# Kernel tuning notes

Measured on AMD Instinct MI355X. Metric: run time of the kernel, lower is better.

The kernel has to match this reference:

```python
import jax, jax.numpy as jnp
import numpy as np


def setup_inputs() -> dict:
    key0 = jax.random.key(0)
    kq, kk, kv = jax.random.split(key0, 3)
    B, S, H, KVH, D = 1, 4096, 8, 2, 64
    return {
        "query": jax.random.normal(kq, (B, S, H, D), dtype=jnp.float32),
        "key": jax.random.normal(kk, (B, S, KVH, D), dtype=jnp.float32),
        "value": jax.random.normal(kv, (B, S, KVH, D), dtype=jnp.float32),
    }


def _ring_attn_single(query, key, value):
    # world_size == 1 (dist uninitialized): ring loop is a single local step
    # with query_offset == key_offset == 0.
    B, S, H, D = query.shape
    KVH = key.shape[2]
    scale = D ** -0.5
    # [B, H, S, D]
    q = query.transpose(0, 2, 1, 3)
    k = key.transpose(0, 2, 1, 3)
    v = value.transpose(0, 2, 1, 3)
    if KVH != H:
        rep = H // KVH
        k = jnp.repeat(k, rep, axis=1)  # repeat_interleave on head dim
        v = jnp.repeat(v, rep, axis=1)
    logits = jnp.einsum("bhqd,bhkd->bhqk", q, k) * scale
    pos = jnp.arange(S)
    causal = pos[:, None] < pos[None, :]  # mask future keys
    logits = jnp.where(causal[None, None], -jnp.inf, logits)
    w = jax.nn.softmax(logits, axis=-1)  # [B, H, S, S]
    attn_out = jnp.einsum("bhqk,bhkd->bhqd", w, v)
    cw = jnp.sum(w, axis=-1, keepdims=True)  # chunk softmax mass (== 1)
    out = attn_out * cw / (cw + 1e-8)  # weight-accumulation renorm
    return out.transpose(0, 2, 1, 3)  # [B, S, H, D]


def reference(query, key, value):
    return _ring_attn_single(query, key, value)
```

## Files before the change

kernel.cpp:

```cpp
#include <hip/hip_runtime.h>
#include <hip/hip_bf16.h>


#define S_LEN 4096
#define H_Q   8
#define H_KV  2
#define DH    64
#define BN    64
#define PITCH 72
#define NEG_BIG (-1e30f)
#define CS (0.125f * 1.44269504088896340736f)

#define CHUNK 12
#define NTR   102
#define KB_SH (S_LEN * H_KV * DH)
#define OB_FLOATS ((size_t)NTR * H_Q * 128 * DH)
#define L_FLOATS  ((size_t)NTR * H_Q * 128)
#define WS_NEED ((size_t)(2 * KB_SH) * 2 + (OB_FLOATS + L_FLOATS) * 4)

typedef __attribute__((ext_vector_type(8))) short bf16x8;
typedef __attribute__((ext_vector_type(4))) short s16x4;
typedef __attribute__((ext_vector_type(4))) float f32x4;
typedef __attribute__((ext_vector_type(4))) unsigned int u32x4;

__device__ __forceinline__ short bf(float x) {
    return __builtin_bit_cast(short, __float2bfloat16(x));
}
__device__ __forceinline__ unsigned int pk2(float lo, float hi) {
    return (unsigned int)(unsigned short)bf(lo)
         | ((unsigned int)(unsigned short)bf(hi) << 16);
}

__global__ __launch_bounds__(256)
void ring_attn_prepass(const float* __restrict__ K, const float* __restrict__ V,
                       short* __restrict__ Kb, short* __restrict__ Vt) {
    const int b = blockIdx.x;
    const int t = threadIdx.x;
    if (b < 512) {
        const int i = (b * 256 + t) * 4;
        float4 kv = *(const float4*)(K + i);
        *(unsigned int*)(Kb + i)     = pk2(kv.x, kv.y);
        *(unsigned int*)(Kb + i + 2) = pk2(kv.z, kv.w);
    } else {
        __shared__ short T[DH * PITCH];
        const int bb  = b - 512;
        const int kvh = bb >> 6;
        const int s0  = (bb & 63) * 64;
        {
            const int r  = t >> 2;
            const int dq = (t & 3) * 16;
            const float* vp = V + ((s0 + r) * H_KV + kvh) * DH + dq;
            float4 a0 = *(const float4*)(vp);
            float4 a1 = *(const float4*)(vp + 4);
            float4 a2 = *(const float4*)(vp + 8);
            float4 a3 = *(const float4*)(vp + 12);
            float e[16] = {a0.x,a0.y,a0.z,a0.w, a1.x,a1.y,a1.z,a1.w,
                           a2.x,a2.y,a2.z,a2.w, a3.x,a3.y,a3.z,a3.w};
#pragma unroll
            for (int i = 0; i < 16; ++i)
                T[(dq + i) * PITCH + r] = bf(e[i]);
        }
        __syncthreads();
        {
            const int d = t >> 2;
            const int q = t & 3;
            s16x4 g0 = *(const s16x4*)(&T[d * PITCH + 4 * q]);
            s16x4 g1 = *(const s16x4*)(&T[d * PITCH + 16 + 4 * q]);
            s16x4 g2 = *(const s16x4*)(&T[d * PITCH + 32 + 4 * q]);
            s16x4 g3 = *(const s16x4*)(&T[d * PITCH + 48 + 4 * q]);
            bf16x8 x0 = bf16x8{g0[0],g0[1],g0[2],g0[3], g1[0],g1[1],g1[2],g1[3]};
            bf16x8 x1 = bf16x8{g2[0],g2[1],g2[2],g2[3], g3[0],g3[1],g3[2],g3[3]};
            short* op = Vt + (kvh * DH + d) * S_LEN + s0 + 16 * q;
            *(bf16x8*)(op)     = x0;
            *(bf16x8*)(op + 8) = x1;
        }
    }
}

template <bool SPLIT>
__global__ __launch_bounds__(256, 4)
void ring_attn_fwd(const float* __restrict__ Q, const short* __restrict__ Kb,
                   const short* __restrict__ Vt, float* __restrict__ O,
                   float* __restrict__ Obuf, float* __restrict__ Lbuf) {
    const int bid = blockIdx.x;
    const int h   = bid & 7;
    int qt, nch, jbeg, jend, tr0;
    if (SPLIT) {
        const int tr = (NTR - 1) - (bid >> 3);
        int b, base;
        if (tr < 6)       { b = 0; base = 0; }
        else if (tr < 18) { b = 1; base = 6; }
        else if (tr < 36) { b = 2; base = 18; }
        else if (tr < 60) { b = 3; base = 36; }
        else if (tr < 90) { b = 4; base = 60; }
        else              { b = 5; base = 90; }
        const int u  = tr - base;
        const int qq = u / (b + 1);
        const int ch = u - qq * (b + 1);
        qt   = 6 * b + qq;
        nch  = b + 1;
        tr0  = base + qq * (b + 1);
        jbeg = ch * CHUNK;
        jend = min(2 * qt + 2, jbeg + CHUNK);
    } else {
        qt = 31 - (bid >> 3);
        nch = 1; jbeg = 0; jend = 2 * qt + 2; tr0 = 0;
    }
    const int kvh = h >> 2;

    __shared__ short Ks[BN * PITCH];
    __shared__ short Vs[DH * PITCH];

    const int tid  = threadIdx.x;
    const int w    = tid >> 6;
    const int lane = tid & 63;
    const int c    = lane & 15;
    const int q    = lane >> 4;

    bf16x8 qf[2][2];
#pragma unroll
    for (int st = 0; st < 2; ++st) {
        const int qg = qt * 128 + st * 64 + w * 16 + c;
        const float* qp = Q + (qg * H_Q + h) * DH + q * 8;
        float4 a0 = *(const float4*)(qp);
        float4 a1 = *(const float4*)(qp + 4);
        float4 b0 = *(const float4*)(qp + 32);
        float4 b1 = *(const float4*)(qp + 36);
        qf[st][0] = bf16x8{bf(a0.x*CS), bf(a0.y*CS), bf(a0.z*CS), bf(a0.w*CS),
                           bf(a1.x*CS), bf(a1.y*CS), bf(a1.z*CS), bf(a1.w*CS)};
        qf[st][1] = bf16x8{bf(b0.x*CS), bf(b0.y*CS), bf(b0.z*CS), bf(b0.w*CS),
                           bf(b1.x*CS), bf(b1.y*CS), bf(b1.z*CS), bf(b1.w*CS)};
    }

    f32x4 acc[2][4] = {};
    float l_lane[2] = {0.f, 0.f};

    const int rr = tid >> 3;
    const int cc = (tid & 7) * 8;

    for (int j = jbeg; j < jend; ++j) {
        __syncthreads();
#pragma unroll
        for (int p = 0; p < 2; ++p) {
            const int n = p * 32 + rr;
            bf16x8 x = *(const bf16x8*)(Kb + ((j * BN + n) * H_KV + kvh) * DH + cc);
            *(bf16x8*)(&Ks[n * PITCH + cc]) = x;
        }
#pragma unroll
        for (int p = 0; p < 2; ++p) {
            const int d = p * 32 + rr;
            bf16x8 x = *(const bf16x8*)(Vt + (kvh * DH + d) * S_LEN + j * BN + cc);
            *(bf16x8*)(&Vs[d * PITCH + cc]) = x;
        }
        __syncthreads();

        bf16x8 pf[2][2];
#pragma unroll
        for (int st = 0; st < 2; ++st) {
            f32x4 s[4] = {};
#pragma unroll
            for (int nt = 0; nt < 4; ++nt) {
                bf16x8 kf0 = *(const bf16x8*)(&Ks[(nt * 16 + c) * PITCH + q * 8]);
                bf16x8 kf1 = *(const bf16x8*)(&Ks[(nt * 16 + c) * PITCH + q * 8 + 32]);
                s[nt] = __builtin_amdgcn_mfma_f32_16x16x32_bf16(kf0, qf[st][0], s[nt], 0, 0, 0);
                s[nt] = __builtin_amdgcn_mfma_f32_16x16x32_bf16(kf1, qf[st][1], s[nt], 0, 0, 0);
            }
            if (j >= 2 * qt + st) {
                const int koff = (j - 2 * qt - st) * 64;
                const int qrl  = w * 16 + c;
#pragma unroll
                for (int nt = 0; nt < 4; ++nt) {
                    const int kl = koff + nt * 16 + q * 4;
#pragma unroll
                    for (int r = 0; r < 4; ++r)
                        if (kl + r > qrl) s[nt][r] = NEG_BIG;
                }
            }
#pragma unroll
            for (int nt = 0; nt < 4; ++nt)
#pragma unroll
                for (int r = 0; r < 4; ++r) {
                    const float p = exp2f(s[nt][r]);
                    s[nt][r] = p;
                    l_lane[st] += p;
                }
            u32x4 w0 = {pk2(s[0][0], s[0][1]), pk2(s[0][2], s[0][3]),
                        pk2(s[1][0], s[1][1]), pk2(s[1][2], s[1][3])};
            u32x4 w1 = {pk2(s[2][0], s[2][1]), pk2(s[2][2], s[2][3]),
                        pk2(s[3][0], s[3][1]), pk2(s[3][2], s[3][3])};
            pf[st][0] = __builtin_bit_cast(bf16x8, w0);
            pf[st][1] = __builtin_bit_cast(bf16x8, w1);
        }

#pragma unroll
        for (int dt = 0; dt < 4; ++dt) {
            const int base = (dt * 16 + c) * PITCH + 16 * q;
            bf16x8 vf0 = *(const bf16x8*)(&Vs[base]);
            bf16x8 vf1 = *(const bf16x8*)(&Vs[base + 8]);
            acc[0][dt] = __builtin_amdgcn_mfma_f32_16x16x32_bf16(pf[0][0], vf0, acc[0][dt], 0, 0, 0);
            acc[0][dt] = __builtin_amdgcn_mfma_f32_16x16x32_bf16(pf[0][1], vf1, acc[0][dt], 0, 0, 0);
            acc[1][dt] = __builtin_amdgcn_mfma_f32_16x16x32_bf16(pf[1][0], vf0, acc[1][dt], 0, 0, 0);
            acc[1][dt] = __builtin_amdgcn_mfma_f32_16x16x32_bf16(pf[1][1], vf1, acc[1][dt], 0, 0, 0);
        }
    }

    float lr[2][4];
#pragma unroll
    for (int st = 0; st < 2; ++st) {
        float t2 = l_lane[st];
        t2 += __shfl_xor(t2, 16);
        t2 += __shfl_xor(t2, 32);
        l_lane[st] = t2;
#pragma unroll
        for (int r = 0; r < 4; ++r)
            lr[st][r] = __shfl(t2, q * 4 + r);
    }

    if (!SPLIT || nch == 1) {
#pragma unroll
        for (int st = 0; st < 2; ++st)
#pragma unroll
            for (int r = 0; r < 4; ++r) {
                const float inv = 1.0f / lr[st][r];
                const int row = qt * 128 + st * 64 + w * 16 + q * 4 + r;
                float* op = O + (row * H_Q + h) * DH + c;
#pragma unroll
                for (int dt = 0; dt < 4; ++dt)
                    op[dt * 16] = acc[st][dt][r] * inv;
            }
    } else {
        const int slot = (tr0 + jbeg / CHUNK) * 8 + h;
        float* ob = Obuf + (size_t)slot * (128 * DH);
#pragma unroll
        for (int st = 0; st < 2; ++st) {
#pragma unroll
            for (int r = 0; r < 4; ++r) {
                const int rin = st * 64 + w * 16 + q * 4 + r;
#pragma unroll
                for (int dt = 0; dt < 4; ++dt)
                    ob[rin * DH + dt * 16 + c] = acc[st][dt][r];
            }
            if (lane < 16)
                Lbuf[slot * 128 + st * 64 + w * 16 + lane] = l_lane[st];
        }
    }
}

__global__ __launch_bounds__(256)
void ring_attn_combine(const float* __restrict__ Obuf, const float* __restrict__ Lbuf,
                       float* __restrict__ O) {
    const int gid  = blockIdx.x * 256 + threadIdx.x;
    const int d    = gid & 63;
    const int h    = (gid >> 6) & 7;
    const int srow = 768 + (gid >> 9);
    const int qt   = srow >> 7;
    const int rin  = srow & 127;
    int b, base;
    if (qt < 12)      { b = 1; base = 6; }
    else if (qt < 18) { b = 2; base = 18; }
    else if (qt < 24) { b = 3; base = 36; }
    else if (qt < 30) { b = 4; base = 60; }
    else              { b = 5; base = 90; }
    const int nch = b + 1;
    const int tr0 = base + (qt - 6 * b) * nch;

    float num = 0.0f, den = 0.0f;
    for (int ch = 0; ch < nch; ++ch) {
        const int slot = (tr0 + ch) * 8 + h;
        den += Lbuf[slot * 128 + rin];
        num += Obuf[(size_t)slot * (128 * DH) + rin * DH + d];
    }
    O[(srow * H_Q + h) * DH + d] = num / den;
}

extern "C" void kernel_launch(void* const* d_in, const int* in_sizes, int n_in,
                              void* d_out, int out_size, void* d_ws, size_t ws_size,
                              hipStream_t stream) {
    const float* Q = (const float*)d_in[0];
    const float* K = (const float*)d_in[1];
    const float* V = (const float*)d_in[2];
    float* O  = (float*)d_out;
    short* Kb = (short*)d_ws;
    short* Vt = Kb + KB_SH;
    float* Obuf = (float*)(Vt + KB_SH);
    float* Lbuf = Obuf + OB_FLOATS;

    ring_attn_prepass<<<640, 256, 0, stream>>>(K, V, Kb, Vt);
    if (ws_size >= WS_NEED) {
        ring_attn_fwd<true><<<NTR * H_Q, 256, 0, stream>>>(Q, Kb, Vt, O, Obuf, Lbuf);
        ring_attn_combine<<<(S_LEN - 768) * H_Q * DH / 256, 256, 0, stream>>>(Obuf, Lbuf, O);
    } else {
        ring_attn_fwd<false><<<32 * H_Q, 256, 0, stream>>>(Q, Kb, Vt, O, Obuf, Lbuf);
    }
}
```

Baseline: 116.5 us.

## Halve split-K chunk size, prefetch K/V tiles, bf16 partial outputs, interleave QK MFMAs

Cuts the split-KV chunk from 12 to 6 key tiles with a new grouping of three query tiles per group. This raises the number of work items from 102 to 187 per head, which should balance load better across CUs. K/V global loads for the next tile are prefetched into registers before the current tile is computed. The QK MFMAs for both query sub-tiles are interleaved. Partial outputs are stored as bf16 to halve workspace traffic, at the cost of extra combine work over more rows and reduced precision in the partial sums.

```diff
diff --git a/kernel.cpp b/kernel.cpp
--- a/kernel.cpp
+++ b/kernel.cpp
@@ -11,12 +11,12 @@
 #define NEG_BIG (-1e30f)
 #define CS (0.125f * 1.44269504088896340736f)
 
-#define CHUNK 12
-#define NTR   102
+#define CHUNK 6
+#define NTR   187
 #define KB_SH (S_LEN * H_KV * DH)
-#define OB_FLOATS ((size_t)NTR * H_Q * 128 * DH)
-#define L_FLOATS  ((size_t)NTR * H_Q * 128)
-#define WS_NEED ((size_t)(2 * KB_SH) * 2 + (OB_FLOATS + L_FLOATS) * 4)
+#define OB_SH    ((size_t)NTR * H_Q * 128 * DH)
+#define L_FLOATS ((size_t)NTR * H_Q * 128)
+#define WS_NEED ((size_t)(2 * KB_SH) * 2 + OB_SH * 2 + L_FLOATS * 4)
 
 typedef __attribute__((ext_vector_type(8))) short bf16x8;
 typedef __attribute__((ext_vector_type(4))) short s16x4;
@@ -25,6 +25,9 @@
 
 __device__ __forceinline__ short bf(float x) {
     return __builtin_bit_cast(short, __float2bfloat16(x));
+}
+__device__ __forceinline__ float fbf(short u) {
+    return __builtin_bit_cast(float, ((unsigned int)(unsigned short)u) << 16);
 }
 __device__ __forceinline__ unsigned int pk2(float lo, float hi) {
     return (unsigned int)(unsigned short)bf(lo)
@@ -81,25 +84,24 @@
 __global__ __launch_bounds__(256, 4)
 void ring_attn_fwd(const float* __restrict__ Q, const short* __restrict__ Kb,
                    const short* __restrict__ Vt, float* __restrict__ O,
-                   float* __restrict__ Obuf, float* __restrict__ Lbuf) {
+                   short* __restrict__ Obuf, float* __restrict__ Lbuf) {
     const int bid = blockIdx.x;
     const int h   = bid & 7;
     int qt, nch, jbeg, jend, tr0;
     if (SPLIT) {
         const int tr = (NTR - 1) - (bid >> 3);
-        int b, base;
-        if (tr < 6)       { b = 0; base = 0; }
-        else if (tr < 18) { b = 1; base = 6; }
-        else if (tr < 36) { b = 2; base = 18; }
-        else if (tr < 60) { b = 3; base = 36; }
-        else if (tr < 90) { b = 4; base = 60; }
-        else              { b = 5; base = 90; }
+        int g = 0, base = 0;
+        for (;;) {
+            const int cnt2 = ((g == 10) ? 2 : 3) * (g + 1);
+            if (tr < base + cnt2) break;
+            base += cnt2; ++g;
+        }
         const int u  = tr - base;
-        const int qq = u / (b + 1);
-        const int ch = u - qq * (b + 1);
-        qt   = 6 * b + qq;
-        nch  = b + 1;
-        tr0  = base + qq * (b + 1);
+        const int qq = u / (g + 1);
+        const int ch = u - qq * (g + 1);
+        qt   = 3 * g + qq;
+        nch  = g + 1;
+        tr0  = base + qq * (g + 1);
         jbeg = ch * CHUNK;
         jend = min(2 * qt + 2, jbeg + CHUNK);
     } else {
@@ -138,33 +140,45 @@
     const int rr = tid >> 3;
     const int cc = (tid & 7) * 8;
 
+    const int kstep = BN * H_KV * DH;
+    const short* kp0 = Kb + (((jbeg * BN) + rr) * H_KV + kvh) * DH + cc;
+    const short* kp1 = kp0 + 32 * H_KV * DH;
+    const short* vp0 = Vt + (kvh * DH + rr) * S_LEN + jbeg * BN + cc;
+    const short* vp1 = vp0 + 32 * S_LEN;
+    bf16x8 kr0 = *(const bf16x8*)kp0;
+    bf16x8 kr1 = *(const bf16x8*)kp1;
+    bf16x8 vr0 = *(const bf16x8*)vp0;
+    bf16x8 vr1 = *(const bf16x8*)vp1;
+
     for (int j = jbeg; j < jend; ++j) {
         __syncthreads();
-#pragma unroll
-        for (int p = 0; p < 2; ++p) {
-            const int n = p * 32 + rr;
-            bf16x8 x = *(const bf16x8*)(Kb + ((j * BN + n) * H_KV + kvh) * DH + cc);
-            *(bf16x8*)(&Ks[n * PITCH + cc]) = x;
-        }
-#pragma unroll
-        for (int p = 0; p < 2; ++p) {
-            const int d = p * 32 + rr;
-            bf16x8 x = *(const bf16x8*)(Vt + (kvh * DH + d) * S_LEN + j * BN + cc);
-            *(bf16x8*)(&Vs[d * PITCH + cc]) = x;
+        *(bf16x8*)(&Ks[rr * PITCH + cc])        = kr0;
+        *(bf16x8*)(&Ks[(32 + rr) * PITCH + cc]) = kr1;
+        *(bf16x8*)(&Vs[rr * PITCH + cc])        = vr0;
+        *(bf16x8*)(&Vs[(32 + rr) * PITCH + cc]) = vr1;
+        if (j + 1 < jend) {
+            kp0 += kstep; kp1 += kstep; vp0 += BN; vp1 += BN;
+            kr0 = *(const bf16x8*)kp0;
+            kr1 = *(const bf16x8*)kp1;
+            vr0 = *(const bf16x8*)vp0;
+            vr1 = *(const bf16x8*)vp1;
         }
         __syncthreads();
 
+        f32x4 s[2][4] = {};
+#pragma unroll
+        for (int nt = 0; nt < 4; ++nt) {
+            bf16x8 kf0 = *(const bf16x8*)(&Ks[(nt * 16 + c) * PITCH + q * 8]);
+            bf16x8 kf1 = *(const bf16x8*)(&Ks[(nt * 16 + c) * PITCH + q * 8 + 32]);
+            s[0][nt] = __builtin_amdgcn_mfma_f32_16x16x32_bf16(kf0, qf[0][0], s[0][nt], 0, 0, 0);
+            s[0][nt] = __builtin_amdgcn_mfma_f32_16x16x32_bf16(kf1, qf[0][1], s[0][nt], 0, 0, 0);
+            s[1][nt] = __builtin_amdgcn_mfma_f32_16x16x32_bf16(kf0, qf[1][0], s[1][nt], 0, 0, 0);
+            s[1][nt] = __builtin_amdgcn_mfma_f32_16x16x32_bf16(kf1, qf[1][1], s[1][nt], 0, 0, 0);
+        }
+
         bf16x8 pf[2][2];
 #pragma unroll
         for (int st = 0; st < 2; ++st) {
-            f32x4 s[4] = {};
-#pragma unroll
-            for (int nt = 0; nt < 4; ++nt) {
-                bf16x8 kf0 = *(const bf16x8*)(&Ks[(nt * 16 + c) * PITCH + q * 8]);
-                bf16x8 kf1 = *(const bf16x8*)(&Ks[(nt * 16 + c) * PITCH + q * 8 + 32]);
-                s[nt] = __builtin_amdgcn_mfma_f32_16x16x32_bf16(kf0, qf[st][0], s[nt], 0, 0, 0);
-                s[nt] = __builtin_amdgcn_mfma_f32_16x16x32_bf16(kf1, qf[st][1], s[nt], 0, 0, 0);
-            }
             if (j >= 2 * qt + st) {
                 const int koff = (j - 2 * qt - st) * 64;
                 const int qrl  = w * 16 + c;
@@ -173,30 +187,30 @@
                     const int kl = koff + nt * 16 + q * 4;
 #pragma unroll
                     for (int r = 0; r < 4; ++r)
-                        if (kl + r > qrl) s[nt][r] = NEG_BIG;
+                        if (kl + r > qrl) s[st][nt][r] = NEG_BIG;
                 }
             }
 #pragma unroll
             for (int nt = 0; nt < 4; ++nt)
 #pragma unroll
                 for (int r = 0; r < 4; ++r) {
-                    const float p = exp2f(s[nt][r]);
-                    s[nt][r] = p;
+                    const float p = exp2f(s[st][nt][r]);
+                    s[st][nt][r] = p;
                     l_lane[st] += p;
                 }
-            u32x4 w0 = {pk2(s[0][0], s[0][1]), pk2(s[0][2], s[0][3]),
-                        pk2(s[1][0], s[1][1]), pk2(s[1][2], s[1][3])};
-            u32x4 w1 = {pk2(s[2][0], s[2][1]), pk2(s[2][2], s[2][3]),
-                        pk2(s[3][0], s[3][1]), pk2(s[3][2], s[3][3])};
+            u32x4 w0 = {pk2(s[st][0][0], s[st][0][1]), pk2(s[st][0][2], s[st][0][3]),
+                        pk2(s[st][1][0], s[st][1][1]), pk2(s[st][1][2], s[st][1][3])};
+            u32x4 w1 = {pk2(s[st][2][0], s[st][2][1]), pk2(s[st][2][2], s[st][2][3]),
+                        pk2(s[st][3][0], s[st][3][1]), pk2(s[st][3][2], s[st][3][3])};
             pf[st][0] = __builtin_bit_cast(bf16x8, w0);
             pf[st][1] = __builtin_bit_cast(bf16x8, w1);
         }
 
 #pragma unroll
         for (int dt = 0; dt < 4; ++dt) {
-            const int base = (dt * 16 + c) * PITCH + 16 * q;
-            bf16x8 vf0 = *(const bf16x8*)(&Vs[base]);
-            bf16x8 vf1 = *(const bf16x8*)(&Vs[base + 8]);
+            const int base2 = (dt * 16 + c) * PITCH + 16 * q;
+            bf16x8 vf0 = *(const bf16x8*)(&Vs[base2]);
+            bf16x8 vf1 = *(const bf16x8*)(&Vs[base2 + 8]);
             acc[0][dt] = __builtin_amdgcn_mfma_f32_16x16x32_bf16(pf[0][0], vf0, acc[0][dt], 0, 0, 0);
             acc[0][dt] = __builtin_amdgcn_mfma_f32_16x16x32_bf16(pf[0][1], vf1, acc[0][dt], 0, 0, 0);
             acc[1][dt] = __builtin_amdgcn_mfma_f32_16x16x32_bf16(pf[1][0], vf0, acc[1][dt], 0, 0, 0);
@@ -230,7 +244,7 @@
             }
     } else {
         const int slot = (tr0 + jbeg / CHUNK) * 8 + h;
-        float* ob = Obuf + (size_t)slot * (128 * DH);
+        short* ob = Obuf + (size_t)slot * (128 * DH);
 #pragma unroll
         for (int st = 0; st < 2; ++st) {
 #pragma unroll
@@ -238,7 +252,7 @@
                 const int rin = st * 64 + w * 16 + q * 4 + r;
 #pragma unroll
                 for (int dt = 0; dt < 4; ++dt)
-                    ob[rin * DH + dt * 16 + c] = acc[st][dt][r];
+                    ob[rin * DH + dt * 16 + c] = bf(acc[st][dt][r]);
             }
             if (lane < 16)
                 Lbuf[slot * 128 + st * 64 + w * 16 + lane] = l_lane[st];
@@ -247,28 +261,24 @@
 }
 
 __global__ __launch_bounds__(256)
-void ring_attn_combine(const float* __restrict__ Obuf, const float* __restrict__ Lbuf,
+void ring_attn_combine(const short* __restrict__ Obuf, const float* __restrict__ Lbuf,
                        float* __restrict__ O) {
     const int gid  = blockIdx.x * 256 + threadIdx.x;
     const int d    = gid & 63;
     const int h    = (gid >> 6) & 7;
-    const int srow = 768 + (gid >> 9);
+    const int srow = 384 + (gid >> 9);
     const int qt   = srow >> 7;
     const int rin  = srow & 127;
-    int b, base;
-    if (qt < 12)      { b = 1; base = 6; }
-    else if (qt < 18) { b = 2; base = 18; }
-    else if (qt < 24) { b = 3; base = 36; }
-    else if (qt < 30) { b = 4; base = 60; }
-    else              { b = 5; base = 90; }
-    const int nch = b + 1;
-    const int tr0 = base + (qt - 6 * b) * nch;
+    const int g    = qt / 3;
+    const int base = 3 * g * (g + 1) / 2;
+    const int nch  = g + 1;
+    const int tr0  = base + (qt - 3 * g) * nch;
 
     float num = 0.0f, den = 0.0f;
     for (int ch = 0; ch < nch; ++ch) {
         const int slot = (tr0 + ch) * 8 + h;
         den += Lbuf[slot * 128 + rin];
-        num += Obuf[(size_t)slot * (128 * DH) + rin * DH + d];
+        num += fbf(Obuf[(size_t)slot * (128 * DH) + rin * DH + d]);
     }
     O[(srow * H_Q + h) * DH + d] = num / den;
 }
@@ -282,13 +292,13 @@
     float* O  = (float*)d_out;
     short* Kb = (short*)d_ws;
     short* Vt = Kb + KB_SH;
-    float* Obuf = (float*)(Vt + KB_SH);
-    float* Lbuf = Obuf + OB_FLOATS;
+    short* Obuf = Vt + KB_SH;
+    float* Lbuf = (float*)(Obuf + OB_SH);
 
     ring_attn_prepass<<<640, 256, 0, stream>>>(K, V, Kb, Vt);
     if (ws_size >= WS_NEED) {
         ring_attn_fwd<true><<<NTR * H_Q, 256, 0, stream>>>(Q, Kb, Vt, O, Obuf, Lbuf);
-        ring_attn_combine<<<(S_LEN - 768) * H_Q * DH / 256, 256, 0, stream>>>(Obuf, Lbuf, O);
+        ring_attn_combine<<<(S_LEN - 384) * H_Q * DH / 256, 256, 0, stream>>>(Obuf, Lbuf, O);
     } else {
         ring_attn_fwd<false><<<32 * H_Q, 256, 0, stream>>>(Q, Kb, Vt, O, Obuf, Lbuf);
     }
```

New measurement: 115.5 us. No clear change (-0.9%).
